# Kernel optimization log

Measured on AMD Instinct MI355X. Metric: run time of the kernel, lower is better.

## Reference

```python
import jax, jax.numpy as jnp
import numpy as np

PENALTY_PARAM = 0.1
NROWS, NCOLS = 256, 256
BATCH = 512


def setup_inputs() -> dict:
    key = jax.random.key(0)
    Y = jax.random.normal(key, (BATCH, NROWS * NCOLS), dtype=jnp.float32)
    return {"Y": Y}


def reference(Y):
    # Y: [B, nrows*ncols] flattened images
    img = Y.reshape(Y.shape[0], NROWS, NCOLS)  # [B, H, W]
    # vertical neighbor diffs: |y[r,c] - y[r+1,c]| for r < H-1
    vdiff = jnp.abs(img[:, :-1, :] - img[:, 1:, :])
    # horizontal neighbor diffs: |y[r,c] - y[r,c+1]| for c < W-1
    hdiff = jnp.abs(img[:, :, :-1] - img[:, :, 1:])
    abs_grad_sum = vdiff.sum(axis=(1, 2)) + hdiff.sum(axis=(1, 2))  # [B]
    areas = Y.sum(axis=1)  # [B]
    return (areas - PENALTY_PARAM * abs_grad_sum)[:, None]  # [B, 1]
```

## Files before the change

kernel.cpp:

```cpp
#include <hip/hip_runtime.h>

#define NROWS   256
#define NCOLS   256
#define PENALTY 0.1f

__global__ __launch_bounds__(256, 8) void gaau_kernel(const float* __restrict__ Y,
                                                      float* __restrict__ out) {
    const int tid  = threadIdx.x;
    const int lane = tid & 63;
    const int wave = tid >> 6;
    const int b    = blockIdx.x >> 2;
    const int q    = blockIdx.x & 3;
    const int r0   = q * 64 + wave * 16;

    const int S = NCOLS / 4;
    const float4* p = (const float4*)(Y + (size_t)b * (NROWS * NCOLS))
                      + r0 * S + lane;

    float4 w0 = p[0 * S];
    float4 w1 = p[1 * S];
    float4 w2 = p[2 * S];
    float4 w3 = p[3 * S];

    float area = 0.0f, gh = 0.0f, gv = 0.0f;
    float4 prev;

    #pragma unroll
    for (int k = 0; k < 17; ++k) {
        float4 cur = w0;
        if (k < 16) {
            float nx = __shfl_down(cur.x, 1, 64);
            area += (cur.x + cur.y) + (cur.z + cur.w);
            gh   += (fabsf(cur.x - cur.y) + fabsf(cur.y - cur.z)) + fabsf(cur.z - cur.w);
            if (lane < 63) gh += fabsf(cur.w - nx);
        }
        if (k > 0) {
            gv += (fabsf(prev.x - cur.x) + fabsf(prev.y - cur.y)) +
                  (fabsf(prev.z - cur.z) + fabsf(prev.w - cur.w));
        }
        prev = cur;
        w0 = w1; w1 = w2; w2 = w3;
        if (k + 4 < 17) {
            if (r0 + k + 4 < NROWS) w3 = p[(k + 4) * S];
        }
    }

    float val = area - PENALTY * (gh + gv);

    #pragma unroll
    for (int off = 32; off > 0; off >>= 1)
        val += __shfl_down(val, off, 64);

    if (lane == 0) atomicAdd(out + b, val);
}

extern "C" void kernel_launch(void* const* d_in, const int* in_sizes, int n_in,
                              void* d_out, int out_size, void* d_ws, size_t ws_size,
                              hipStream_t stream) {
    const float* Y  = (const float*)d_in[0];
    float* out      = (float*)d_out;
    const int batch = in_sizes[0] / (NROWS * NCOLS);
    gaau_kernel<<<batch * 4, 256, 0, stream>>>(Y, out);
}
```

Measured before the change: 207.8 us.

## Split each image into eight row bands and preload all rows upfront

Doubles the grid so each wave handles 8 rows instead of 16. All nine rows (including the halo) are loaded into registers before computing, replacing the rolling 4-deep prefetch window. Launch bounds are relaxed to 4 blocks per CU. This raises memory-level parallelism and block count, at the cost of more halo re-reads and twice as many atomics.

```diff
diff --git a/kernel.cpp b/kernel.cpp
--- a/kernel.cpp
+++ b/kernel.cpp
@@ -4,45 +4,38 @@
 #define NCOLS   256
 #define PENALTY 0.1f
 
-__global__ __launch_bounds__(256, 8) void gaau_kernel(const float* __restrict__ Y,
+__global__ __launch_bounds__(256, 4) void gaau_kernel(const float* __restrict__ Y,
                                                       float* __restrict__ out) {
     const int tid  = threadIdx.x;
     const int lane = tid & 63;
     const int wave = tid >> 6;
-    const int b    = blockIdx.x >> 2;
-    const int q    = blockIdx.x & 3;
-    const int r0   = q * 64 + wave * 16;
+    const int b    = blockIdx.x >> 3;
+    const int band = blockIdx.x & 7;
+    const int r0   = band * 32 + wave * 8;
 
     const int S = NCOLS / 4;
     const float4* p = (const float4*)(Y + (size_t)b * (NROWS * NCOLS))
                       + r0 * S + lane;
 
-    float4 w0 = p[0 * S];
-    float4 w1 = p[1 * S];
-    float4 w2 = p[2 * S];
-    float4 w3 = p[3 * S];
+    float4 v[9];
+    #pragma unroll
+    for (int k = 0; k < 8; ++k) v[k] = p[k * S];
+    v[8] = (r0 + 8 < NROWS) ? p[8 * S] : v[7];
+
+    float nx[8];
+    #pragma unroll
+    for (int k = 0; k < 8; ++k) nx[k] = __shfl_down(v[k].x, 1, 64);
 
     float area = 0.0f, gh = 0.0f, gv = 0.0f;
-    float4 prev;
-
     #pragma unroll
-    for (int k = 0; k < 17; ++k) {
-        float4 cur = w0;
-        if (k < 16) {
-            float nx = __shfl_down(cur.x, 1, 64);
-            area += (cur.x + cur.y) + (cur.z + cur.w);
-            gh   += (fabsf(cur.x - cur.y) + fabsf(cur.y - cur.z)) + fabsf(cur.z - cur.w);
-            if (lane < 63) gh += fabsf(cur.w - nx);
-        }
-        if (k > 0) {
-            gv += (fabsf(prev.x - cur.x) + fabsf(prev.y - cur.y)) +
-                  (fabsf(prev.z - cur.z) + fabsf(prev.w - cur.w));
-        }
-        prev = cur;
-        w0 = w1; w1 = w2; w2 = w3;
-        if (k + 4 < 17) {
-            if (r0 + k + 4 < NROWS) w3 = p[(k + 4) * S];
-        }
+    for (int k = 0; k < 8; ++k) {
+        float4 c = v[k];
+        area += (c.x + c.y) + (c.z + c.w);
+        gh   += (fabsf(c.x - c.y) + fabsf(c.y - c.z)) + fabsf(c.z - c.w);
+        if (lane < 63) gh += fabsf(c.w - nx[k]);
+        float4 n = v[k + 1];
+        gv += (fabsf(c.x - n.x) + fabsf(c.y - n.y)) +
+              (fabsf(c.z - n.z) + fabsf(c.w - n.w));
     }
 
     float val = area - PENALTY * (gh + gv);
@@ -52,6 +45,7 @@
         val += __shfl_down(val, off, 64);
 
     if (lane == 0) atomicAdd(out + b, val);
+
 }
 
 extern "C" void kernel_launch(void* const* d_in, const int* in_sizes, int n_in,
@@ -60,5 +54,5 @@
     const float* Y  = (const float*)d_in[0];
     float* out      = (float*)d_out;
     const int batch = in_sizes[0] / (NROWS * NCOLS);
-    gaau_kernel<<<batch * 4, 256, 0, stream>>>(Y, out);
+    gaau_kernel<<<batch * 8, 256, 0, stream>>>(Y, out);
 }
```

Result: slower. 212.2 us (+2.1%).
